# Kernel optimization log

Hardware: AMD Instinct MI355X
Metric: run time of the kernel (lower is better)

Reference implementation:

```python
import jax, jax.numpy as jnp
import numpy as np

N, F, M, E = 8192, 256, 128, 131072


def setup_inputs() -> dict:
    key = jax.random.key(0)
    k = jax.random.split(key, 6)
    x = jax.random.normal(k[0], (N, F), dtype=jnp.float32)
    edge_index = jax.random.randint(k[1], (2, E), 0, N, dtype=jnp.int64)
    eps = jax.random.normal(k[2], (N, M), dtype=jnp.float32)
    # small init scale so sigmoid(z_i . z_j) isn't saturated
    W_mu = jax.random.normal(k[3], (F, M), dtype=jnp.float32) * 0.05
    b_mu = jnp.zeros((M,), dtype=jnp.float32)
    W_sig = jax.random.normal(k[4], (F, M), dtype=jnp.float32) * 0.05
    b_sig = jnp.zeros((M,), dtype=jnp.float32)
    return {"x": x, "edge_index": edge_index, "eps": eps,
            "W_mu": W_mu, "b_mu": b_mu, "W_sig": W_sig, "b_sig": b_sig}


def reference(x, edge_index, eps, W_mu, b_mu, W_sig, b_sig):
    # Gaussian encoder: Normal(mu, exp(logstd)), Independent over latent dim
    mu = x @ W_mu + b_mu                      # [N, M]
    logstd = x @ W_sig + b_sig                # [N, M]
    sigma = jnp.exp(logstd)
    z = mu + sigma * eps                      # rsample, [N, M]

    # decoder.probability(dot(z_i, z_j)) = sigmoid(logit); vectorized as Z @ Z.T
    logits = z @ z.T                          # [N, N]

    # symmetric adjacency labels from edge_index (either direction counts)
    src, dst = edge_index[0], edge_index[1]
    adj = jnp.zeros((N, N), dtype=jnp.float32)
    adj = adj.at[src, dst].set(1.0)
    adj = adj.at[dst, src].set(1.0)

    # BCE(sigmoid(s), y) summed over unordered pairs i < j (stable logits form)
    per_pair = jax.nn.softplus(logits) - adj * logits  # = -[y log p + (1-y) log(1-p)]
    triu = jnp.triu(jnp.ones((N, N), dtype=bool), k=1)
    bce = jnp.sum(jnp.where(triu, per_pair, 0.0))

    # sum_i KL( N(mu_i, sigma_i) || N(0, I) )
    kl = jnp.sum(0.5 * (sigma * sigma + mu * mu - 1.0) - logstd)

    return bce + 0.001 * kl
```

## Files before the change

### kernel.cpp

```cpp
#include <hip/hip_runtime.h>

#define NN 8192
#define FF 256
#define MM 128
#define HSLOTS 262144

typedef __attribute__((ext_vector_type(8))) short bf16x8;
typedef __attribute__((ext_vector_type(4))) float f32x4;

#define P_KL    0
#define P_EDGE  (64 * 16)
#define P_SP    (128 * 16)
#define Z_OFF   16384
#define Z_BYTES (NN * MM * 2)
#define HASH_OFF (Z_OFF + Z_BYTES)
#define WT_OFF  (HASH_OFF + HSLOTS * 4)
#define WT_BYTES (MM * FF * 2)
#define ZF_OFF  (WT_OFF + 2 * WT_BYTES)

__device__ __forceinline__ float wave_reduce(float v) {
    #pragma unroll
    for (int off = 32; off > 0; off >>= 1) v += __shfl_down(v, off);
    return v;
}
__device__ __forceinline__ unsigned short f2bf(float f) {
    unsigned int u = __float_as_uint(f);
    u += 0x7fffu + ((u >> 16) & 1u);
    return (unsigned short)(u >> 16);
}
__device__ __forceinline__ int4 pack8(float4 a, float4 b) {
    int4 p;
    p.x = (int)f2bf(a.x) | ((int)f2bf(a.y) << 16);
    p.y = (int)f2bf(a.z) | ((int)f2bf(a.w) << 16);
    p.z = (int)f2bf(b.x) | ((int)f2bf(b.y) << 16);
    p.w = (int)f2bf(b.z) | ((int)f2bf(b.w) << 16);
    return p;
}

__global__ __launch_bounds__(256)
void prep_w(const float* __restrict__ Wmu, const float* __restrict__ Wsg,
            unsigned short* __restrict__ WmuT, unsigned short* __restrict__ WsgT,
            float* __restrict__ part, unsigned int* __restrict__ ht) {
    const int t = blockIdx.x * 256 + threadIdx.x;
    const int n = t >> 8, f = t & 255;
    WmuT[t] = f2bf(Wmu[f * MM + n]);
    WsgT[t] = f2bf(Wsg[f * MM + n]);
    if (t < 4096) part[t] = 0.f;
    uint4 z4 = {0u, 0u, 0u, 0u};
    ((uint4*)ht)[t * 2]     = z4;
    ((uint4*)ht)[t * 2 + 1] = z4;
}

#define XP_I4 33
#define XP_S  264

__global__ __launch_bounds__(256)
void encoder_mfma(const float* __restrict__ x, const float* __restrict__ eps,
                  const unsigned short* __restrict__ WmuT,
                  const unsigned short* __restrict__ WsgT,
                  const float* __restrict__ bmu, const float* __restrict__ bsg,
                  unsigned short* __restrict__ zb, unsigned short* __restrict__ zf,
                  float* __restrict__ part) {
    __shared__ int4 ax[16 * XP_I4];
    __shared__ float red[4];
    const int tid = threadIdx.x;
    const int wid = tid >> 6, lane = tid & 63;
    const int l15 = lane & 15, quad = lane >> 4;
    const int row0 = blockIdx.x * 16;

    {
        const int r = tid >> 4, ch = tid & 15;
        const float4* g0 = (const float4*)(x + (size_t)(row0 + r) * FF + ch * 8);
        const float4* g1 = (const float4*)(x + (size_t)(row0 + r) * FF + (ch + 16) * 8);
        ax[r * XP_I4 + ch]      = pack8(g0[0], g0[1]);
        ax[r * XP_I4 + ch + 16] = pack8(g1[0], g1[1]);
    }
    __syncthreads();

    const short* sax = (const short*)ax;
    const int4* wtm = (const int4*)WmuT;
    const int4* wts = (const int4*)WsgT;

    f32x4 zero4 = {0.f, 0.f, 0.f, 0.f};
    f32x4 accm[2], accl[2];
    accm[0] = accm[1] = accl[0] = accl[1] = zero4;

    #pragma unroll
    for (int ks = 0; ks < 8; ++ks) {
        const bf16x8 a = *(const bf16x8*)&sax[l15 * XP_S + ks * 32 + quad * 8];
        #pragma unroll
        for (int j = 0; j < 2; ++j) {
            const int n = wid * 32 + j * 16 + l15;
            const bf16x8 bmf = *(const bf16x8*)&wtm[n * 32 + ks * 4 + quad];
            const bf16x8 bsf = *(const bf16x8*)&wts[n * 32 + ks * 4 + quad];
            accm[j] = __builtin_amdgcn_mfma_f32_16x16x32_bf16(a, bmf, accm[j], 0, 0, 0);
            accl[j] = __builtin_amdgcn_mfma_f32_16x16x32_bf16(a, bsf, accl[j], 0, 0, 0);
        }
    }

    const int rt = row0 >> 4;
    float klp = 0.f;
    #pragma unroll
    for (int j = 0; j < 2; ++j) {
        const int col = wid * 32 + j * 16 + l15;
        const float bm = bmu[col], bs = bsg[col];
        const int kq = col >> 3, c7 = col & 7;
        #pragma unroll
        for (int r = 0; r < 4; ++r) {
            const int row = row0 + quad * 4 + r;
            const float mu = accm[j][r] + bm;
            const float ls = accl[j][r] + bs;
            const float sg = __expf(ls);
            const float zz = fmaf(sg, eps[(size_t)row * MM + col], mu);
            const unsigned short zv = f2bf(zz);
            zb[(size_t)row * MM + col] = zv;
            zf[(size_t)(((rt * 16 + kq) * 16) + quad * 4 + r) * 8 + c7] = zv;
            klp += 0.5f * (sg * sg + mu * mu - 1.f) - ls;
        }
    }

    klp = wave_reduce(klp);
    if (lane == 0) red[wid] = klp;
    __syncthreads();
    if (tid == 0)
        atomicAdd(&part[P_KL + (blockIdx.x & 63) * 16],
                  red[0] + red[1] + red[2] + red[3]);
}

__device__ __forceinline__ float dotpair(unsigned int a, unsigned int b) {
    const float al = __uint_as_float(a << 16);
    const float ah = __uint_as_float(a & 0xffff0000u);
    const float bl = __uint_as_float(b << 16);
    const float bh = __uint_as_float(b & 0xffff0000u);
    return fmaf(al, bl, ah * bh);
}

__global__ __launch_bounds__(256)
void fused_kernel(const int* __restrict__ ei, int E, int eblocks,
                  const unsigned short* __restrict__ zb,
                  const unsigned short* __restrict__ zf,
                  unsigned int* __restrict__ ht, float* __restrict__ part) {
    const int tid = threadIdx.x;
    const int wid = tid >> 6, lane = tid & 63;
    const int l15 = lane & 15, quad = lane >> 4;

    if ((int)blockIdx.x < eblocks) {
        const int g = lane >> 4;
        const int base0 = blockIdx.x * 128 + wid * 32;
        float accum = 0.f;
        #pragma unroll 2
        for (int p = 0; p < 8; ++p) {
            const int e = base0 + p * 4 + g;
            float s = 0.f;
            int i = 0, j = 0, a = 0, b = 0;
            if (e < E) {
                i = ei[e];
                j = ei[E + e];
                a = min(i, j); b = max(i, j);
                const uint4 ua = ((const uint4*)(zb + (size_t)a * MM))[l15];
                const uint4 ub = ((const uint4*)(zb + (size_t)b * MM))[l15];
                s = dotpair(ua.x, ub.x) + dotpair(ua.y, ub.y)
                  + dotpair(ua.z, ub.z) + dotpair(ua.w, ub.w);
            }
            s += __shfl_down(s, 8);
            s += __shfl_down(s, 4);
            s += __shfl_down(s, 2);
            s += __shfl_down(s, 1);
            if (l15 == 0 && e < E && i != j) {
                const unsigned int key = (unsigned int)a * NN + b;
                unsigned int slot = (key * 2654435761u) & (HSLOTS - 1);
                bool first = false;
                for (;;) {
                    const unsigned int old = atomicCAS(&ht[slot], 0u, key);
                    if (old == 0u) { first = true; break; }
                    if (old == key) break;
                    slot = (slot + 1) & (HSLOTS - 1);
                }
                if (first) accum += s;
            }
        }
        accum = wave_reduce(accum);
        if (lane == 0)
            atomicAdd(&part[P_EDGE + ((blockIdx.x * 4 + wid) & 63) * 16], accum);
        return;
    }

    const int q = blockIdx.x - eblocks;
    int bi = (int)((129.0f - sqrtf(fmaxf(129.0f * 129.0f - 8.0f * (float)q, 0.f))) * 0.5f);
    bi = max(0, min(bi, 63));
    while ((bi + 1) * (129 - (bi + 1)) / 2 <= q && bi < 63) ++bi;
    while (bi * (129 - bi) / 2 > q) --bi;
    const int bj = bi + (q - bi * (129 - bi) / 2);

    const int wm = wid >> 1, wn = wid & 1;
    const bf16x8* zv = (const bf16x8*)zf;
    const int art = bi * 8 + wm * 4;
    const int brt = bj * 8 + wn * 4;

    f32x4 zero4 = {0.f, 0.f, 0.f, 0.f};
    f32x4 acc[4][4];
    #pragma unroll
    for (int i = 0; i < 4; ++i)
        #pragma unroll
        for (int j = 0; j < 4; ++j) acc[i][j] = zero4;

    bf16x8 aA[4], bA[4], aB[4], bB[4];
    #define LOADF(dstA, dstB, ks)                                             \
        _Pragma("unroll")                                                     \
        for (int t = 0; t < 4; ++t) {                                         \
            dstA[t] = zv[((art + t) * 16 + (ks) * 4 + quad) * 16 + l15];      \
            dstB[t] = zv[((brt + t) * 16 + (ks) * 4 + quad) * 16 + l15];      \
        }
    #define MFMAS(srcA, srcB)                                                 \
        _Pragma("unroll")                                                     \
        for (int i = 0; i < 4; ++i)                                           \
            _Pragma("unroll")                                                 \
            for (int j = 0; j < 4; ++j)                                       \
                acc[i][j] = __builtin_amdgcn_mfma_f32_16x16x32_bf16(          \
                    srcA[i], srcB[j], acc[i][j], 0, 0, 0);

    LOADF(aA, bA, 0)
    LOADF(aB, bB, 1)
    MFMAS(aA, bA)
    LOADF(aA, bA, 2)
    MFMAS(aB, bB)
    LOADF(aB, bB, 3)
    MFMAS(aA, bA)
    MFMAS(aB, bB)
    #undef LOADF
    #undef MFMAS

    float tsum = 0.f;
    if (bi != bj) {
        #pragma unroll
        for (int i = 0; i < 4; ++i)
            #pragma unroll
            for (int j = 0; j < 4; ++j)
                #pragma unroll
                for (int r = 0; r < 4; ++r) {
                    const float v = acc[i][j][r];
                    const float e = __expf(-fabsf(v));
                    tsum += fmaxf(v, 0.f) + e * fmaf(e, -0.5f, 1.f);
                }
    } else {
        const int rbase = wm * 64 + quad * 4;
        const int cbase = wn * 64 + l15;
        #pragma unroll
        for (int i = 0; i < 4; ++i)
            #pragma unroll
            for (int j = 0; j < 4; ++j)
                #pragma unroll
                for (int r = 0; r < 4; ++r)
                    if (cbase + j * 16 > rbase + i * 16 + r) {
                        const float v = acc[i][j][r];
                        const float e = __expf(-fabsf(v));
                        tsum += fmaxf(v, 0.f) + e * fmaf(e, -0.5f, 1.f);
                    }
    }

    tsum = wave_reduce(tsum);
    if (lane == 0)
        atomicAdd(&part[P_SP + ((q * 4 + wid) & 63) * 16], tsum);
}

__global__ void combine_kernel(const float* __restrict__ part,
                               float* __restrict__ out) {
    const int t = threadIdx.x;
    float v = part[P_SP + t * 16] - part[P_EDGE + t * 16]
            + 0.001f * part[P_KL + t * 16];
    v = wave_reduce(v);
    if (t == 0) out[0] = v;
}

extern "C" void kernel_launch(void* const* d_in, const int* in_sizes, int n_in,
                              void* d_out, int out_size, void* d_ws, size_t ws_size,
                              hipStream_t stream) {
    const float* x   = (const float*)d_in[0];
    const int* ei    = (const int*)d_in[1];
    const float* eps = (const float*)d_in[2];
    const float* Wmu = (const float*)d_in[3];
    const float* bmu = (const float*)d_in[4];
    const float* Wsg = (const float*)d_in[5];
    const float* bsg = (const float*)d_in[6];
    float* out = (float*)d_out;
    char* ws = (char*)d_ws;

    float* part = (float*)ws;
    unsigned short* zb = (unsigned short*)(ws + Z_OFF);
    unsigned int* ht = (unsigned int*)(ws + HASH_OFF);
    unsigned short* WmuT = (unsigned short*)(ws + WT_OFF);
    unsigned short* WsgT = (unsigned short*)(ws + WT_OFF + WT_BYTES);
    unsigned short* zf = (unsigned short*)(ws + ZF_OFF);
    const int E = in_sizes[1] / 2;
    const int eblocks = (E + 127) / 128;

    prep_w<<<128, 256, 0, stream>>>(Wmu, Wsg, WmuT, WsgT, part, ht);
    encoder_mfma<<<NN / 16, 256, 0, stream>>>(x, eps, WmuT, WsgT, bmu, bsg,
                                              zb, zf, part);
    fused_kernel<<<eblocks + 2080, 256, 0, stream>>>(ei, E, eblocks, zb, zf,
                                                     ht, part);
    combine_kernel<<<1, 64, 0, stream>>>(part, out);
}
```

Baseline: 132.2 us.

## Pair triangle tiles per block, dedupe edges before gathers, fold combine into last block

New measurement: 220.9 us. 1.67x slower.

```diff
diff --git a/kernel.cpp b/kernel.cpp
--- a/kernel.cpp
+++ b/kernel.cpp
@@ -11,12 +11,15 @@
 #define P_KL    0
 #define P_EDGE  (64 * 16)
 #define P_SP    (128 * 16)
+#define CNT_IDX 3072
 #define Z_OFF   16384
 #define Z_BYTES (NN * MM * 2)
 #define HASH_OFF (Z_OFF + Z_BYTES)
 #define WT_OFF  (HASH_OFF + HSLOTS * 4)
 #define WT_BYTES (MM * FF * 2)
 #define ZF_OFF  (WT_OFF + 2 * WT_BYTES)
+
+#define TBLOCKS 1056
 
 __device__ __forceinline__ float wave_reduce(float v) {
     #pragma unroll
@@ -136,140 +139,156 @@
 }
 
 __global__ __launch_bounds__(256)
-void fused_kernel(const int* __restrict__ ei, int E, int eblocks,
+void fused_kernel(const int* __restrict__ ei, int E,
                   const unsigned short* __restrict__ zb,
                   const unsigned short* __restrict__ zf,
-                  unsigned int* __restrict__ ht, float* __restrict__ part) {
+                  unsigned int* __restrict__ ht, float* __restrict__ part,
+                  float* __restrict__ out) {
     const int tid = threadIdx.x;
     const int wid = tid >> 6, lane = tid & 63;
     const int l15 = lane & 15, quad = lane >> 4;
 
-    if ((int)blockIdx.x < eblocks) {
+    if ((int)blockIdx.x < TBLOCKS) {
+        int q = blockIdx.x;
+        int bi = 0, P = 32;
+        while (q >= P) { q -= P; ++bi; P = (65 - bi) >> 1; }
+        const int bj0 = bi + 2 * q;
+        const int ntile = (bj0 < 63) ? 2 : 1;
+
+        const int wm = wid >> 1, wn = wid & 1;
+        const bf16x8* zv = (const bf16x8*)zf;
+        const int art = bi * 8 + wm * 4;
+
+        float tsum = 0.f;
+        for (int t = 0; t < ntile; ++t) {
+            const int bj = bj0 + t;
+            const int brt = bj * 8 + wn * 4;
+
+            f32x4 zero4 = {0.f, 0.f, 0.f, 0.f};
+            f32x4 acc[4][4];
+            #pragma unroll
+            for (int i = 0; i < 4; ++i)
+                #pragma unroll
+                for (int j = 0; j < 4; ++j) acc[i][j] = zero4;
+
+            bf16x8 aA[4], bA[4], aB[4], bB[4];
+            #define LOADF(dstA, dstB, ks)                                         \
+                _Pragma("unroll")                                                 \
+                for (int u = 0; u < 4; ++u) {                                     \
+                    dstA[u] = zv[((art + u) * 16 + (ks) * 4 + quad) * 16 + l15];  \
+                    dstB[u] = zv[((brt + u) * 16 + (ks) * 4 + quad) * 16 + l15];  \
+                }
+            #define MFMAS(srcA, srcB)                                             \
+                _Pragma("unroll")                                                 \
+                for (int i = 0; i < 4; ++i)                                       \
+                    _Pragma("unroll")                                             \
+                    for (int j = 0; j < 4; ++j)                                   \
+                        acc[i][j] = __builtin_amdgcn_mfma_f32_16x16x32_bf16(      \
+                            srcA[i], srcB[j], acc[i][j], 0, 0, 0);
+
+            LOADF(aA, bA, 0)
+            LOADF(aB, bB, 1)
+            MFMAS(aA, bA)
+            LOADF(aA, bA, 2)
+            MFMAS(aB, bB)
+            LOADF(aB, bB, 3)
+            MFMAS(aA, bA)
+            MFMAS(aB, bB)
+            #undef LOADF
+            #undef MFMAS
+
+            if (bi != bj) {
+                #pragma unroll
+                for (int i = 0; i < 4; ++i)
+                    #pragma unroll
+                    for (int j = 0; j < 4; ++j)
+                        #pragma unroll
+                        for (int r = 0; r < 4; ++r) {
+                            const float v = acc[i][j][r];
+                            const float e = __expf(-fabsf(v));
+                            tsum += fmaxf(v, 0.f) + e * fmaf(e, -0.5f, 1.f);
+                        }
+            } else {
+                const int rbase = wm * 64 + quad * 4;
+                const int cbase = wn * 64 + l15;
+                #pragma unroll
+                for (int i = 0; i < 4; ++i)
+                    #pragma unroll
+                    for (int j = 0; j < 4; ++j)
+                        #pragma unroll
+                        for (int r = 0; r < 4; ++r)
+                            if (cbase + j * 16 > rbase + i * 16 + r) {
+                                const float v = acc[i][j][r];
+                                const float e = __expf(-fabsf(v));
+                                tsum += fmaxf(v, 0.f) + e * fmaf(e, -0.5f, 1.f);
+                            }
+            }
+        }
+
+        tsum = wave_reduce(tsum);
+        if (lane == 0)
+            atomicAdd(&part[P_SP + ((blockIdx.x * 4 + wid) & 63) * 16], tsum);
+    } else {
+        const int eb = blockIdx.x - TBLOCKS;
+        const int e = eb * 256 + tid;
+        int i = 0, j = 0;
+        if (e < E) { i = ei[e]; j = ei[E + e]; }
+        const int a = min(i, j), b = max(i, j);
+        bool first = false;
+        if (e < E && i != j) {
+            const unsigned int key = (unsigned int)a * NN + b;
+            unsigned int slot = (key * 2654435761u) & (HSLOTS - 1);
+            for (;;) {
+                const unsigned int old = atomicCAS(&ht[slot], 0u, key);
+                if (old == 0u) { first = true; break; }
+                if (old == key) break;
+                slot = (slot + 1) & (HSLOTS - 1);
+            }
+        }
         const int g = lane >> 4;
-        const int base0 = blockIdx.x * 128 + wid * 32;
-        float accum = 0.f;
-        #pragma unroll 2
-        for (int p = 0; p < 8; ++p) {
-            const int e = base0 + p * 4 + g;
-            float s = 0.f;
-            int i = 0, j = 0, a = 0, b = 0;
-            if (e < E) {
-                i = ei[e];
-                j = ei[E + e];
-                a = min(i, j); b = max(i, j);
-                const uint4 ua = ((const uint4*)(zb + (size_t)a * MM))[l15];
-                const uint4 ub = ((const uint4*)(zb + (size_t)b * MM))[l15];
-                s = dotpair(ua.x, ub.x) + dotpair(ua.y, ub.y)
-                  + dotpair(ua.z, ub.z) + dotpair(ua.w, ub.w);
-            }
+        const unsigned long long m = __ballot(first);
+        unsigned int gm = (unsigned int)((m >> (g * 16)) & 0xffffULL);
+        float gacc = 0.f;
+        while (gm) {
+            const int w = __ffs(gm) - 1;
+            gm &= gm - 1;
+            const int src = (g << 4) | w;
+            const int aw = __shfl(a, src);
+            const int bw = __shfl(b, src);
+            const uint4 ua = ((const uint4*)(zb + (size_t)aw * MM))[l15];
+            const uint4 ub = ((const uint4*)(zb + (size_t)bw * MM))[l15];
+            float s = dotpair(ua.x, ub.x) + dotpair(ua.y, ub.y)
+                    + dotpair(ua.z, ub.z) + dotpair(ua.w, ub.w);
             s += __shfl_down(s, 8);
             s += __shfl_down(s, 4);
             s += __shfl_down(s, 2);
             s += __shfl_down(s, 1);
-            if (l15 == 0 && e < E && i != j) {
-                const unsigned int key = (unsigned int)a * NN + b;
-                unsigned int slot = (key * 2654435761u) & (HSLOTS - 1);
-                bool first = false;
-                for (;;) {
-                    const unsigned int old = atomicCAS(&ht[slot], 0u, key);
-                    if (old == 0u) { first = true; break; }
-                    if (old == key) break;
-                    slot = (slot + 1) & (HSLOTS - 1);
-                }
-                if (first) accum += s;
-            }
-        }
-        accum = wave_reduce(accum);
+            if (l15 == 0) gacc += s;
+        }
+        gacc = wave_reduce(gacc);
         if (lane == 0)
-            atomicAdd(&part[P_EDGE + ((blockIdx.x * 4 + wid) & 63) * 16], accum);
-        return;
-    }
-
-    const int q = blockIdx.x - eblocks;
-    int bi = (int)((129.0f - sqrtf(fmaxf(129.0f * 129.0f - 8.0f * (float)q, 0.f))) * 0.5f);
-    bi = max(0, min(bi, 63));
-    while ((bi + 1) * (129 - (bi + 1)) / 2 <= q && bi < 63) ++bi;
-    while (bi * (129 - bi) / 2 > q) --bi;
-    const int bj = bi + (q - bi * (129 - bi) / 2);
-
-    const int wm = wid >> 1, wn = wid & 1;
-    const bf16x8* zv = (const bf16x8*)zf;
-    const int art = bi * 8 + wm * 4;
-    const int brt = bj * 8 + wn * 4;
-
-    f32x4 zero4 = {0.f, 0.f, 0.f, 0.f};
-    f32x4 acc[4][4];
-    #pragma unroll
-    for (int i = 0; i < 4; ++i)
-        #pragma unroll
-        for (int j = 0; j < 4; ++j) acc[i][j] = zero4;
-
-    bf16x8 aA[4], bA[4], aB[4], bB[4];
-    #define LOADF(dstA, dstB, ks)                                             \
-        _Pragma("unroll")                                                     \
-        for (int t = 0; t < 4; ++t) {                                         \
-            dstA[t] = zv[((art + t) * 16 + (ks) * 4 + quad) * 16 + l15];      \
-            dstB[t] = zv[((brt + t) * 16 + (ks) * 4 + quad) * 16 + l15];      \
-        }
-    #define MFMAS(srcA, srcB)                                                 \
-        _Pragma("unroll")                                                     \
-        for (int i = 0; i < 4; ++i)                                           \
-            _Pragma("unroll")                                                 \
-            for (int j = 0; j < 4; ++j)                                       \
-                acc[i][j] = __builtin_amdgcn_mfma_f32_16x16x32_bf16(          \
-                    srcA[i], srcB[j], acc[i][j], 0, 0, 0);
-
-    LOADF(aA, bA, 0)
-    LOADF(aB, bB, 1)
-    MFMAS(aA, bA)
-    LOADF(aA, bA, 2)
-    MFMAS(aB, bB)
-    LOADF(aB, bB, 3)
-    MFMAS(aA, bA)
-    MFMAS(aB, bB)
-    #undef LOADF
-    #undef MFMAS
-
-    float tsum = 0.f;
-    if (bi != bj) {
-        #pragma unroll
-        for (int i = 0; i < 4; ++i)
-            #pragma unroll
-            for (int j = 0; j < 4; ++j)
-                #pragma unroll
-                for (int r = 0; r < 4; ++r) {
-                    const float v = acc[i][j][r];
-                    const float e = __expf(-fabsf(v));
-                    tsum += fmaxf(v, 0.f) + e * fmaf(e, -0.5f, 1.f);
-                }
-    } else {
-        const int rbase = wm * 64 + quad * 4;
-        const int cbase = wn * 64 + l15;
-        #pragma unroll
-        for (int i = 0; i < 4; ++i)
-            #pragma unroll
-            for (int j = 0; j < 4; ++j)
-                #pragma unroll
-                for (int r = 0; r < 4; ++r)
-                    if (cbase + j * 16 > rbase + i * 16 + r) {
-                        const float v = acc[i][j][r];
-                        const float e = __expf(-fabsf(v));
-                        tsum += fmaxf(v, 0.f) + e * fmaf(e, -0.5f, 1.f);
-                    }
-    }
-
-    tsum = wave_reduce(tsum);
-    if (lane == 0)
-        atomicAdd(&part[P_SP + ((q * 4 + wid) & 63) * 16], tsum);
-}
-
-__global__ void combine_kernel(const float* __restrict__ part,
-                               float* __restrict__ out) {
-    const int t = threadIdx.x;
-    float v = part[P_SP + t * 16] - part[P_EDGE + t * 16]
-            + 0.001f * part[P_KL + t * 16];
-    v = wave_reduce(v);
-    if (t == 0) out[0] = v;
+            atomicAdd(&part[P_EDGE + ((eb * 4 + wid) & 63) * 16], gacc);
+    }
+
+    __shared__ unsigned int lastflag;
+    __threadfence();
+    if (tid == 0) {
+        const unsigned int done =
+            atomicAdd((unsigned int*)&part[CNT_IDX], 1u);
+        lastflag = (done == gridDim.x - 1) ? 1u : 0u;
+    }
+    __syncthreads();
+    if (lastflag && tid < 64) {
+        __threadfence();
+        float v = __hip_atomic_load(&part[P_SP + tid * 16],
+                                    __ATOMIC_RELAXED, __HIP_MEMORY_SCOPE_AGENT)
+                - __hip_atomic_load(&part[P_EDGE + tid * 16],
+                                    __ATOMIC_RELAXED, __HIP_MEMORY_SCOPE_AGENT)
+                + 0.001f * __hip_atomic_load(&part[P_KL + tid * 16],
+                                    __ATOMIC_RELAXED, __HIP_MEMORY_SCOPE_AGENT);
+        v = wave_reduce(v);
+        if (tid == 0) out[0] = v;
+    }
 }
 
 extern "C" void kernel_launch(void* const* d_in, const int* in_sizes, int n_in,
@@ -292,12 +311,11 @@
     unsigned short* WsgT = (unsigned short*)(ws + WT_OFF + WT_BYTES);
     unsigned short* zf = (unsigned short*)(ws + ZF_OFF);
     const int E = in_sizes[1] / 2;
-    const int eblocks = (E + 127) / 128;
+    const int eblocks = (E + 255) / 256;
 
     prep_w<<<128, 256, 0, stream>>>(Wmu, Wsg, WmuT, WsgT, part, ht);
     encoder_mfma<<<NN / 16, 256, 0, stream>>>(x, eps, WmuT, WsgT, bmu, bsg,
                                               zb, zf, part);
-    fused_kernel<<<eblocks + 2080, 256, 0, stream>>>(ei, E, eblocks, zb, zf,
-                                                     ht, part);
-    combine_kernel<<<1, 64, 0, stream>>>(part, out);
-}
+    fused_kernel<<<TBLOCKS + eblocks, 256, 0, stream>>>(ei, E, zb, zf, ht,
+                                                        part, out);
+}
```
